# Optimization experiments

Hardware: AMD Instinct MI355X
Metric: run time of the kernel (lower is better)

## Reference

```python
import jax, jax.numpy as jnp
import numpy as np

N_NODES = 50000
N_EDGES = 800000
MAX_ITER = 20  # torchdeq default f_max_iter=40; fixed iteration count for a tractable jit-able baseline
K = 3          # TAGConv default number of hops
INS, EMB, HID, OUT = 4, 64, 128, 1


def setup_inputs():
    key = jax.random.key(0)
    ks = jax.random.split(key, 12)
    def lin(k, fan_in, fan_out):
        return jax.random.normal(k, (fan_in, fan_out), jnp.float32) / np.sqrt(fan_in)
    def tag_w(k, fan_in, fan_out):
        # stacked weights for the K+1 TAGConv linear maps: [K+1, in, out]
        return jax.random.normal(k, (K + 1, fan_in, fan_out), jnp.float32) / np.sqrt(fan_in * (K + 1))
    return {
        "x": jax.random.normal(ks[0], (N_NODES, INS), jnp.float32),
        "pos": jax.random.normal(ks[1], (N_NODES, 3), jnp.float32),
        "edge_attr": jax.random.uniform(ks[2], (N_EDGES,), jnp.float32),
        "up_w1": lin(ks[3], INS, EMB), "up_b1": jnp.zeros((EMB,), jnp.float32),
        "up_w2": lin(ks[4], EMB, EMB), "up_b2": jnp.zeros((EMB,), jnp.float32),
        "c1_w": tag_w(ks[5], EMB + 3, HID), "c1_b": jnp.zeros((HID,), jnp.float32),
        "c2_w": tag_w(ks[6], HID, HID), "c2_b": jnp.zeros((HID,), jnp.float32),
        "c3_w": tag_w(ks[7], HID, EMB), "c3_b": jnp.zeros((EMB,), jnp.float32),
        "down_w1": lin(ks[8], EMB, OUT), "down_b1": jnp.zeros((OUT,), jnp.float32),
        "down_w2": lin(ks[9], OUT, OUT), "down_b2": jnp.zeros((OUT,), jnp.float32),
        "edge_index": jax.random.randint(ks[10], (2, N_EDGES), 0, N_NODES, jnp.int32),
    }


def _gcn_norm(row, col, edge_attr, n):
    # PyG gcn_norm with edge weights, no self loops (TAGConv default)
    deg = jax.ops.segment_sum(edge_attr, col, num_segments=n)
    safe = jnp.where(deg > 0, deg, 1.0)
    dinv = jnp.where(deg > 0, jax.lax.rsqrt(safe), 0.0)
    return dinv[row] * edge_attr * dinv[col]


def _mlp(x, w1, b1, w2, b2):
    # torch F.gelu default = exact erf gelu
    return jax.nn.gelu(x @ w1 + b1, approximate=False) @ w2 + b2


def reference(x, pos, edge_attr, up_w1, up_b1, up_w2, up_b2, c1_w, c1_b, c2_w, c2_b, c3_w, c3_b, down_w1, down_b1, down_w2, down_b2, edge_index):
    n = x.shape[0]
    row, col = edge_index[0], edge_index[1]
    norm = _gcn_norm(row, col, edge_attr, n)

    def tag(h, W, b):
        # TAGConv: sum_k lin_k( A_hat^k x ) + bias
        out = h @ W[0]
        for k in range(1, W.shape[0]):
            h = jax.ops.segment_sum(h[row] * norm[:, None], col, num_segments=n)  # [E,C] gather-scatter
            out = out + h @ W[k]
        return out + b

    def gnn(z):
        h = jnp.concatenate([z, pos], axis=1)
        h = jax.nn.relu(tag(h, c1_w, c1_b))
        h = jax.nn.relu(tag(h, c2_w, c2_b))  # F.dropout is identity in eval mode
        h = tag(h, c3_w, c3_b)
        return jax.nn.log_softmax(h, axis=1)

    z0 = _mlp(x, up_w1, up_b1, up_w2, up_b2)
    z = jax.lax.fori_loop(0, MAX_ITER, lambda i, zz: gnn(zz), z0)  # fixed-point solver
    z_star = gnn(z)  # phantom-gradient step (torchdeq grad=1)
    out = _mlp(z_star, down_w1, down_b1, down_w2, down_b2)
    return out, z_star
```

## Files before the change

kernel.cpp:

```cpp
#include <hip/hip_runtime.h>
#include <hip/hip_bf16.h>

#define N_NODES 50000
#define N_EDGES 800000
#define MAX_ITER 20

typedef __attribute__((ext_vector_type(8))) short bf16x8;
typedef __attribute__((ext_vector_type(4))) float f32x4;
typedef __attribute__((ext_vector_type(2))) float f32x2;
typedef unsigned char uchar;

__device__ __forceinline__ float gelu_f(float x){
  return 0.5f*x*(1.0f+erff(x*0.70710678118654752f));
}
__device__ __forceinline__ ushort f2b(float f){
  uint x = __float_as_uint(f);
  uint r = (x + 0x7fffu + ((x>>16)&1u)) >> 16;
  return (ushort)r;
}

#if __has_builtin(__builtin_amdgcn_cvt_pk_f32_fp8) && __has_builtin(__builtin_amdgcn_cvt_pk_fp8_f32)
#define HW_FP8 1
#endif

__device__ __forceinline__ uint fp8_enc1_sw(float x){
  uint u = __float_as_uint(x);
  uint s = (u>>24)&0x80u;
  int e = (int)((u>>23)&0xffu);
  uint m = u&0x7fffffu;
  uint m3 = (m + 0x80000u)>>20;
  if (m3==8u){ e+=1; m3=0u; }
  int e8 = e-120;
  if (e8<=0) return s;
  if (e8>=15) return s|0x7eu;
  return s | ((uint)e8<<3) | m3;
}
__device__ __forceinline__ float fp8_dec1_sw(uint b){
  uint s=(b&0x80u)<<24;
  uint em=b&0x7fu;
  if (em==0u) return __uint_as_float(s);
  if ((em>>3)==0u) return (s?-1.f:1.f)*(float)em*0.001953125f;
  return __uint_as_float(s | ((em+960u)<<20));
}
__device__ __forceinline__ void fp8_dec8(uint lo, uint hi, float* d){
#ifdef HW_FP8
  f32x2 a = __builtin_amdgcn_cvt_pk_f32_fp8(lo,false);
  f32x2 b = __builtin_amdgcn_cvt_pk_f32_fp8(lo,true);
  f32x2 c = __builtin_amdgcn_cvt_pk_f32_fp8(hi,false);
  f32x2 e = __builtin_amdgcn_cvt_pk_f32_fp8(hi,true);
  d[0]=a[0];d[1]=a[1];d[2]=b[0];d[3]=b[1];d[4]=c[0];d[5]=c[1];d[6]=e[0];d[7]=e[1];
#else
  d[0]=fp8_dec1_sw(lo&0xffu);        d[1]=fp8_dec1_sw((lo>>8)&0xffu);
  d[2]=fp8_dec1_sw((lo>>16)&0xffu);  d[3]=fp8_dec1_sw(lo>>24);
  d[4]=fp8_dec1_sw(hi&0xffu);        d[5]=fp8_dec1_sw((hi>>8)&0xffu);
// ... 128 lines not shown
  float acc2 = sb2[c];
  #pragma unroll 8
  for (int k=0;k<64;k++) acc2 += t1s[g][k]*sw2[k*64+c];
  z[(size_t)node*64+c] = f2b(acc2);
  z8[(size_t)node*64+c] = fp8_enc1(acc2);
}

template<int LDIN>
__global__ void posprop(const float* __restrict__ in, float* __restrict__ out,
                        const int* __restrict__ starts, const int* __restrict__ crow,
                        const float* __restrict__ cnrm){
  int v = blockIdx.x*256+threadIdx.x;
  if (v >= N_NODES) return;
  int s=starts[v], e=starts[v+1];
  float a0=0.f,a1=0.f,a2=0.f;
  for (int i=s;i<e;++i){
    int r=crow[i]; float nm=cnrm[i];
    a0 = fmaf(in[(size_t)r*LDIN+0], nm, a0);
    a1 = fmaf(in[(size_t)r*LDIN+1], nm, a1);
    a2 = fmaf(in[(size_t)r*LDIN+2], nm, a2);
  }
  float4 o = {a0,a1,a2,0.f};
  *(float4*)(out + (size_t)v*4) = o;
}

__global__ __launch_bounds__(256) void posbias_kernel(
    const float* __restrict__ pos, const float* __restrict__ P1,
    const float* __restrict__ P2, const float* __restrict__ P3,
    const float* __restrict__ c1w, const float* __restrict__ c1b,
    ushort* __restrict__ pb){
  __shared__ float sw[4][3][128];
  int tid=threadIdx.x;
  for (int i=tid; i<4*3*128; i+=256){
    int cc=i&127; int d=(i>>7)%3; int j=i/(3*128);
    sw[j][d][cc] = c1w[((size_t)j*67 + 64 + d)*128 + cc];
  }
  __syncthreads();
  int idx = blockIdx.x*256+tid;
  if (idx < N_NODES*128){
    int n = idx>>7, cc = idx&127;
    float a = c1b[cc];
    #pragma unroll
    for (int d=0;d<3;d++) a = fmaf(pos[(size_t)n*3+d], sw[0][d][cc], a);
    #pragma unroll
    for (int d=0;d<3;d++) a = fmaf(P1[(size_t)n*4+d], sw[1][d][cc], a);
    #pragma unroll
    for (int d=0;d<3;d++) a = fmaf(P2[(size_t)n*4+d], sw[2][d][cc], a);
    #pragma unroll
    for (int d=0;d<3;d++) a = fmaf(P3[(size_t)n*4+d], sw[3][d][cc], a);
    pb[idx]=f2b(a);
  }
}

template<int MODE, bool IN8, bool OUT8>
__global__ __launch_bounds__(256) void prop64k(
    const void* __restrict__ hin, ushort* __restrict__ obf,
    uchar* __restrict__ of8, float* __restrict__ of32,
    const ushort* __restrict__ adj, const float* __restrict__ bias,
    const int* __restrict__ starts, const int* __restrict__ crow,
    const float* __restrict__ cnrm){
  constexpr bool WBF = (MODE==0) || (MODE==2) || (MODE==1 && !OUT8);
  int wv = threadIdx.x >> 6;
  int v = blockIdx.x*4 + wv;
  int t = threadIdx.x & 63;
  int g = t >> 3;
  int c = t & 7;
  int s = starts[v], e = starts[v+1];
  float acc[8] = {0,0,0,0,0,0,0,0};
  for (int i=s; i<e; i+=64){
    int cnt = e - i; if (cnt > 64) cnt = 64;
    int r = 0; float nm = 0.f;
    if (t < cnt){ r = crow[i+t]; nm = cnrm[i+t]; }
    for (int jb=0; jb<cnt; jb+=8){
      int rr = __shfl(r, jb+g, 64);
      float nmj = __shfl(nm, jb+g, 64);
      float hv[8];
      if (IN8){
        uint2 d = *(const uint2*)((const uchar*)hin + (size_t)rr*64 + c*8);
        fp8_dec8(d.x, d.y, hv);
      } else {
        uint4 d = *(const uint4*)((const ushort*)hin + (size_t)rr*64 + c*8);
        const uint* dp = (const uint*)&d;
        #pragma unroll
        for (int q=0;q<4;q++){
          hv[2*q]   = __uint_as_float(dp[q]<<16);
          hv[2*q+1] = __uint_as_float(dp[q]&0xffff0000u);
        }
      }
      #pragma unroll
      for (int q=0;q<8;q++) acc[q] = fmaf(hv[q], nmj, acc[q]);
    }
  }
  #pragma unroll
  for (int q=0;q<8;q++){
    acc[q] += __shfl_xor(acc[q], 8, 64);
    acc[q] += __shfl_xor(acc[q], 16, 64);
    acc[q] += __shfl_xor(acc[q], 32, 64);
  }
  if (MODE==0 || MODE==1){
    if (g==0){
      float val[8];
      if (MODE==1){
        uint4 av = *(const uint4*)(adj + (size_t)v*64 + c*8);
        const uint* ap=(const uint*)&av;
        #pragma unroll
        for (int q=0;q<4;q++){
          val[2*q]   = acc[2*q]   + __uint_as_float(ap[q]<<16);
          val[2*q+1] = acc[2*q+1] + __uint_as_float(ap[q]&0xffff0000u);
        }
      } else {
        #pragma unroll
        for (int q=0;q<8;q++) val[q]=acc[q];
      }
      if (WBF){
        uint4 o; uint* op=(uint*)&o;
        #pragma unroll
        for (int q=0;q<4;q++) op[q] = (uint)f2b(val[2*q]) | ((uint)f2b(val[2*q+1])<<16);
        *(uint4*)(obf + (size_t)v*64 + c*8) = o;
      }
      if (OUT8){
        uint2 o8;
        o8.x = fp8_enc4(val[0],val[1],val[2],val[3]);
        o8.y = fp8_enc4(val[4],val[5],val[6],val[7]);
        *(uint2*)(of8 + (size_t)v*64 + c*8) = o8;
      }
    }
  } else {
    uint4 av = *(const uint4*)(adj + (size_t)v*64 + c*8);
    const uint* ap=(const uint*)&av;
    float vv[8];
    #pragma unroll
    for (int q=0;q<4;q++){
      vv[2*q]   = acc[2*q]   + __uint_as_float(ap[q]<<16)         + bias[c*8+2*q];
      vv[2*q+1] = acc[2*q+1] + __uint_as_float(ap[q]&0xffff0000u) + bias[c*8+2*q+1];
    }
    float m = vv[0];
    #pragma unroll
    for (int q=1;q<8;q++) m = fmaxf(m, vv[q]);
    m = fmaxf(m, __shfl_xor(m,1,64));
    m = fmaxf(m, __shfl_xor(m,2,64));
    m = fmaxf(m, __shfl_xor(m,4,64));
    float ss = 0.f;
    #pragma unroll
    for (int q=0;q<8;q++) ss += __expf(vv[q]-m);
    ss += __shfl_xor(ss,1,64);
    ss += __shfl_xor(ss,2,64);
    ss += __shfl_xor(ss,4,64);
    float lse = m + __logf(ss);
    if (g==0){
      if (MODE==2){
        uint4 o; uint* op=(uint*)&o;
        #pragma unroll
        for (int q=0;q<4;q++) op[q] = (uint)f2b(vv[2*q]-lse) | ((uint)f2b(vv[2*q+1]-lse)<<16);
        *(uint4*)(obf + (size_t)v*64 + c*8) = o;
        if (OUT8){
          uint2 o8;
          o8.x = fp8_enc4(vv[0]-lse,vv[1]-lse,vv[2]-lse,vv[3]-lse);
          o8.y = fp8_enc4(vv[4]-lse,vv[5]-lse,vv[6]-lse,vv[7]-lse);
          *(uint2*)(of8 + (size_t)v*64 + c*8) = o8;
        }
      } else {
        float* zo = of32 + (size_t)v*64 + c*8;
        float4 o0 = {vv[0]-lse, vv[1]-lse, vv[2]-lse, vv[3]-lse};
        float4 o1 = {vv[4]-lse, vv[5]-lse, vv[6]-lse, vv[7]-lse};
        *(float4*)zo = o0;
        *(float4*)(zo+4) = o1;
      }
    }
  }
}

template<bool IN8, bool OUT8>
__global__ __launch_bounds__(256) void prop128k(
    const void* __restrict__ hin, ushort* __restrict__ obf,
    uchar* __restrict__ of8,
    const int* __restrict__ starts, const int* __restrict__ crow,
    const float* __restrict__ cnrm){
  int wv = threadIdx.x >> 6;
  int v = blockIdx.x*4 + wv;
  int t = threadIdx.x & 63;
  int g = t >> 4;
  int c = t & 15;
  int s = starts[v], e = starts[v+1];
  float acc[8] = {0,0,0,0,0,0,0,0};
  for (int i=s; i<e; i+=64){
    int cnt = e - i; if (cnt > 64) cnt = 64;
    int r = 0; float nm = 0.f;
    if (t < cnt){ r = crow[i+t]; nm = cnrm[i+t]; }
    for (int jb=0; jb<cnt; jb+=4){
      int rr  = __shfl(r,  jb+g, 64);
      float nmj = __shfl(nm, jb+g, 64);
      float hv[8];
      if (IN8){
        uint2 d = *(const uint2*)((const uchar*)hin + (size_t)rr*128 + c*8);
        fp8_dec8(d.x, d.y, hv);
      } else {
        uint4 d = *(const uint4*)((const ushort*)hin + (size_t)rr*128 + c*8);
        const uint* dp = (const uint*)&d;
        #pragma unroll
        for (int q=0;q<4;q++){
          hv[2*q]   = __uint_as_float(dp[q]<<16);
          hv[2*q+1] = __uint_as_float(dp[q]&0xffff0000u);
        }
      }
      #pragma unroll
      for (int q=0;q<8;q++) acc[q] = fmaf(hv[q], nmj, acc[q]);
    }
  }
  #pragma unroll
  for (int q=0;q<8;q++){
    acc[q] += __shfl_xor(acc[q], 16, 64);
    acc[q] += __shfl_xor(acc[q], 32, 64);
  }
  if (g==0){
    uint4 o; uint* op=(uint*)&o;
    #pragma unroll
    for (int q=0;q<4;q++) op[q] = (uint)f2b(acc[2*q]) | ((uint)f2b(acc[2*q+1])<<16);
    *(uint4*)(obf + (size_t)v*128 + c*8) = o;
    if (OUT8){
      uint2 o8;
      o8.x = fp8_enc4(acc[0],acc[1],acc[2],acc[3]);
      o8.y = fp8_enc4(acc[4],acc[5],acc[6],acc[7]);
      *(uint2*)(of8 + (size_t)v*128 + c*8) = o8;
    }
  }
}

template<int KC, bool PERNODE_BIAS, bool OUT8>
__global__ __launch_bounds__(256) void gemm4in(
    const ushort* __restrict__ H0, const ushort* __restrict__ H1,
    const ushort* __restrict__ H2, const ushort* __restrict__ H3,
    const ushort* __restrict__ PB, const void* __restrict__ biasp,
    ushort* __restrict__ out, uchar* __restrict__ out8){
  constexpr int NT = 8;
  constexpr int NKS = KC/32;
  int lane = threadIdx.x & 63;
  int wv   = threadIdx.x >> 6;
  int m0 = blockIdx.x*64 + wv*16;
  int lr = lane & 15, lg = lane >> 4;
  int arow = m0 + lr; if (arow > N_NODES-1) arow = N_NODES-1;
  const ushort* Hs[4] = {H0,H1,H2,H3};
  f32x4 acc[NT];
  #pragma unroll
  for (int t=0;t<NT;t++) acc[t] = (f32x4){0.f,0.f,0.f,0.f};
  #pragma unroll
  for (int j=0;j<4;j++){
    const ushort* Hj  = Hs[j] + (size_t)arow*KC + lg*8;
    const ushort* PBj = PB + (size_t)j*(KC/8)*128*8;
    #pragma unroll
    for (int ks=0; ks<NKS; ks++){
      bf16x8 af = *(const bf16x8*)(Hj + ks*32);
      int kb = ks*4 + lg;
      #pragma unroll
      for (int t=0;t<NT;t++){
        bf16x8 bf = *(const bf16x8*)(PBj + ((size_t)kb*128 + t*16 + lr)*8);
        acc[t] = __builtin_amdgcn_mfma_f32_16x16x32_bf16(af, bf, acc[t], 0, 0, 0);
      }
    }
  }
  #pragma unroll
  for (int t=0;t<NT;t++){
    #pragma unroll
    for (int q=0;q<4;q++){
      int node = m0 + lg*4 + q;
      if (node < N_NODES){
        int col = t*16 + lr;
        float b;
        if (PERNODE_BIAS) b = __uint_as_float(((uint)((const ushort*)biasp)[(size_t)node*128+col])<<16);
        else              b = ((const float*)biasp)[col];
        float vo = fmaxf(acc[t][q] + b, 0.f);
        out[(size_t)node*128 + col] = f2b(vo);
        if (OUT8) out8[(size_t)node*128 + col] = fp8_enc1(vo);
      }
    }
  }
}

__global__ __launch_bounds__(256) void gemm_y(
    const ushort* __restrict__ T2, const ushort* __restrict__ PB,
    ushort* __restrict__ Y, uchar* __restrict__ Y3_8){
  constexpr int NT = 16;
  int lane = threadIdx.x & 63;
  int wv   = threadIdx.x >> 6;
  int m0 = blockIdx.x*64 + wv*16;
  int lr = lane & 15, lg = lane >> 4;
  int arow = m0 + lr; if (arow > N_NODES-1) arow = N_NODES-1;
  f32x4 acc[NT];
  #pragma unroll
  for (int t=0;t<NT;t++) acc[t] = (f32x4){0.f,0.f,0.f,0.f};
  const ushort* Hj = T2 + (size_t)arow*128 + lg*8;
  #pragma unroll
  for (int ks=0; ks<4; ks++){
    bf16x8 af = *(const bf16x8*)(Hj + ks*32);
    int kb = ks*4 + lg;
    #pragma unroll
    for (int t=0;t<NT;t++){
      bf16x8 bf = *(const bf16x8*)(PB + ((size_t)kb*256 + t*16 + lr)*8);
      acc[t] = __builtin_amdgcn_mfma_f32_16x16x32_bf16(af, bf, acc[t], 0, 0, 0);
    }
  }
  #pragma unroll
  for (int t=0;t<NT;t++){
    int n = t*16 + lr;
    int j = n >> 6, cc = n & 63;
    #pragma unroll
    for (int q=0;q<4;q++){
      int node = m0 + lg*4 + q;
      if (node < N_NODES){
        Y[(size_t)j*N_NODES*64 + (size_t)node*64 + cc] = f2b(acc[t][q]);
        if (j==3) Y3_8[(size_t)node*64 + cc] = fp8_enc1(acc[t][q]);
      }
    }
  }
}

__global__ __launch_bounds__(256) void mlp_down_kernel(
    const float* __restrict__ zs, const float* __restrict__ dw1, const float* __restrict__ db1,
    const float* __restrict__ dw2, const float* __restrict__ db2, float* __restrict__ out){
  int node = blockIdx.x*4 + (threadIdx.x>>6);
  int c = threadIdx.x & 63;
  float v = zs[(size_t)node*64+c]*dw1[c];
  #pragma unroll
  for (int off=32; off; off>>=1) v += __shfl_xor(v, off, 64);
  if (c==0) out[node] = gelu_f(v + db1[0]) * dw2[0] + db2[0];
}

extern "C" void kernel_launch(void* const* d_in, const int* in_sizes, int n_in,
                              void* d_out, int out_size, void* d_ws, size_t ws_size,
                              hipStream_t stream){
  const float* x     = (const float*)d_in[0];
  const float* pos   = (const float*)d_in[1];
  const float* eattr = (const float*)d_in[2];
  const float* up_w1 = (const float*)d_in[3];
  const float* up_b1 = (const float*)d_in[4];
  const float* up_w2 = (const float*)d_in[5];
  const float* up_b2 = (const float*)d_in[6];
  const float* c1_w  = (const float*)d_in[7];
  const float* c1_b  = (const float*)d_in[8];
  const float* c2_w  = (const float*)d_in[9];
  const float* c2_b  = (const float*)d_in[10];
  const float* c3_w  = (const float*)d_in[11];
  const float* c3_b  = (const float*)d_in[12];
  const float* dw1   = (const float*)d_in[13];
  const float* db1   = (const float*)d_in[14];
  const float* dw2   = (const float*)d_in[15];
  const float* db2   = (const float*)d_in[16];
  const int*   eidx  = (const int*)d_in[17];
  const int* row = eidx;
  const int* col = eidx + N_EDGES;

  char* wsp = (char*)d_ws;
  size_t off = 0;
  auto alloc = [&](size_t bytes)->char*{
    char* p = wsp + off;
    off = (off + bytes + 255) & ~(size_t)255;
    return p;
  };
  float*  deg    = (float*)alloc((size_t)N_NODES*4);
  int*    cnt    = (int*)  alloc((size_t)N_NODES*4);
  int*    starts = (int*)  alloc((size_t)(N_NODES+1)*4);
  int*    cursor = (int*)  alloc((size_t)N_NODES*4);
  float*  nrm    = (float*)alloc((size_t)N_EDGES*4);
  int*    crow   = (int*)  alloc((size_t)N_EDGES*4);
  float*  cnrm   = (float*)alloc((size_t)N_EDGES*4);
  float*  P1     = (float*)alloc((size_t)N_NODES*4*4);
  float*  P2     = (float*)alloc((size_t)N_NODES*4*4);
  float*  P3     = (float*)alloc((size_t)N_NODES*4*4);
  ushort* pbias  = (ushort*)alloc((size_t)N_NODES*128*2);
  ushort* z      = (ushort*)alloc((size_t)N_NODES*64*2);
  ushort* q1     = (ushort*)alloc((size_t)N_NODES*64*2);
  ushort* q2     = (ushort*)alloc((size_t)N_NODES*64*2);
  ushort* q3     = (ushort*)alloc((size_t)N_NODES*64*2);
  ushort* t1     = (ushort*)alloc((size_t)N_NODES*128*2);
  ushort* p1     = (ushort*)alloc((size_t)N_NODES*128*2);
  ushort* p2     = (ushort*)alloc((size_t)N_NODES*128*2);
  ushort* p3     = (ushort*)alloc((size_t)N_NODES*128*2);
  ushort* t2     = (ushort*)alloc((size_t)N_NODES*128*2);
  ushort* PB1    = (ushort*)alloc((size_t)4*8*128*8*2);
  ushort* PB2    = (ushort*)alloc((size_t)4*16*128*8*2);
  ushort* PB3    = (ushort*)alloc((size_t)16*256*8*2);
  uchar*  z8     = (uchar*)alloc((size_t)N_NODES*64);
  uchar*  q1_8   = (uchar*)alloc((size_t)N_NODES*64);
  uchar*  q2_8   = (uchar*)alloc((size_t)N_NODES*64);
  uchar*  t1_8   = (uchar*)alloc((size_t)N_NODES*128);
  uchar*  p1_8   = (uchar*)alloc((size_t)N_NODES*128);
  uchar*  p2_8   = (uchar*)alloc((size_t)N_NODES*128);
  uchar*  Y3_8   = (uchar*)alloc((size_t)N_NODES*64);
  uchar*  u1_8   = (uchar*)alloc((size_t)N_NODES*64);
  uchar*  u2_8   = (uchar*)alloc((size_t)N_NODES*64);

  ushort* Y  = p1;
  ushort* Y0 = Y;
  ushort* Y1 = Y + (size_t)1*N_NODES*64;
  ushort* Y2 = Y + (size_t)2*N_NODES*64;
  ushort* Y3 = Y + (size_t)3*N_NODES*64;
  ushort* u1 = q1;
  ushort* u2 = q2;

  float* outv  = (float*)d_out;
  float* zstar = (float*)d_out + N_NODES;

  hipMemsetAsync(deg, 0, (size_t)N_NODES*4, stream);
  hipMemsetAsync(cnt, 0, (size_t)N_NODES*4, stream);
  int eb = (N_EDGES+255)/256;
  deg_cnt_kernel<<<eb,256,0,stream>>>(col, eattr, deg, cnt);
  norm_kernel<<<eb,256,0,stream>>>(row, col, eattr, deg, nrm);
  scan_kernel<<<1,1024,0,stream>>>(cnt, starts, cursor);
  fill_kernel<<<eb,256,0,stream>>>(row, col, nrm, cursor, crow, cnrm);
  pack_w1<<<128,256,0,stream>>>(c1_w, PB1);
  pack_w2<<<256,256,0,stream>>>(c2_w, PB2);
  pack_w3<<<128,256,0,stream>>>(c3_w, PB3);
  mlp_up_kernel<<<N_NODES/4,256,0,stream>>>(x, up_w1, up_b1, up_w2, up_b2, z, z8);

  int nb = (N_NODES+255)/256;
  posprop<3><<<nb,256,0,stream>>>(pos, P1, starts, crow, cnrm);
  posprop<4><<<nb,256,0,stream>>>(P1,  P2, starts, crow, cnrm);
  posprop<4><<<nb,256,0,stream>>>(P2,  P3, starts, crow, cnrm);
  posbias_kernel<<<(N_NODES*128)/256,256,0,stream>>>(pos, P1, P2, P3, c1_w, c1_b, pbias);

  const int gprop = N_NODES/4;
  const int ggemm = (N_NODES+63)/64;

  for (int it=0; it<=MAX_ITER; ++it){
    if (it < MAX_ITER){
      prop64k<0,true,true> <<<gprop,256,0,stream>>>(z8,   q1, q1_8, nullptr, nullptr, nullptr, starts, crow, cnrm);
      prop64k<0,true,true> <<<gprop,256,0,stream>>>(q1_8, q2, q2_8, nullptr, nullptr, nullptr, starts, crow, cnrm);
      prop64k<0,true,false><<<gprop,256,0,stream>>>(q2_8, q3, nullptr, nullptr, nullptr, nullptr, starts, crow, cnrm);
      gemm4in<64,true,true><<<ggemm,256,0,stream>>>(z,q1,q2,q3,PB1,pbias,t1,t1_8);

      prop128k<true,true> <<<gprop,256,0,stream>>>(t1_8, p1, p1_8, starts, crow, cnrm);
      prop128k<true,true> <<<gprop,256,0,stream>>>(p1_8, p2, p2_8, starts, crow, cnrm);
      prop128k<true,false><<<gprop,256,0,stream>>>(p2_8, p3, nullptr, starts, crow, cnrm);
      gemm4in<128,false,false><<<ggemm,256,0,stream>>>(t1,p1,p2,p3,PB2,c2_b,t2,nullptr);

      gemm_y<<<ggemm,256,0,stream>>>(t2, PB3, Y, Y3_8);
      prop64k<1,true,true><<<gprop,256,0,stream>>>(Y3_8, nullptr, u1_8, nullptr, Y2, nullptr, starts, crow, cnrm);
      prop64k<1,true,true><<<gprop,256,0,stream>>>(u1_8, nullptr, u2_8, nullptr, Y1, nullptr, starts, crow, cnrm);
      prop64k<2,true,true><<<gprop,256,0,stream>>>(u2_8, z, z8, nullptr, Y0, c3_b, starts, crow, cnrm);
    } else {
      prop64k<0,false,false><<<gprop,256,0,stream>>>(z,  q1, nullptr, nullptr, nullptr, nullptr, starts, crow, cnrm);
      prop64k<0,false,false><<<gprop,256,0,stream>>>(q1, q2, nullptr, nullptr, nullptr, nullptr, starts, crow, cnrm);
      prop64k<0,false,false><<<gprop,256,0,stream>>>(q2, q3, nullptr, nullptr, nullptr, nullptr, starts, crow, cnrm);
      gemm4in<64,true,false><<<ggemm,256,0,stream>>>(z,q1,q2,q3,PB1,pbias,t1,nullptr);

      prop128k<false,false><<<gprop,256,0,stream>>>(t1, p1, nullptr, starts, crow, cnrm);
      prop128k<false,false><<<gprop,256,0,stream>>>(p1, p2, nullptr, starts, crow, cnrm);
      prop128k<false,false><<<gprop,256,0,stream>>>(p2, p3, nullptr, starts, crow, cnrm);
      gemm4in<128,false,false><<<ggemm,256,0,stream>>>(t1,p1,p2,p3,PB2,c2_b,t2,nullptr);

      gemm_y<<<ggemm,256,0,stream>>>(t2, PB3, Y, Y3_8);
      prop64k<1,false,false><<<gprop,256,0,stream>>>(Y3, u1, nullptr, nullptr, Y2, nullptr, starts, crow, cnrm);
      prop64k<1,false,false><<<gprop,256,0,stream>>>(u1, u2, nullptr, nullptr, Y1, nullptr, starts, crow, cnrm);
      prop64k<3,false,false><<<gprop,256,0,stream>>>(u2, nullptr, nullptr, zstar, Y0, c3_b, starts, crow, cnrm);
    }
  }
  mlp_down_kernel<<<N_NODES/4,256,0,stream>>>(zstar, dw1, db1, dw2, db2, outv);
}
```

Before: 6.940 ms.

## Fuse fixed-point iteration into a persistent cooperative megakernel with grid syncs

Replaces the 252 per-stage kernel launches of the fixed-point loop with one cooperative persistent kernel. Each stage becomes a grid-stride device function, and grid.sync() separates the stages, so launch gaps and tail effects between kernels should go away. The grid is capped at 1024 blocks, fewer than the original per-stage grids, so each block loops over several node groups. Occupancy is limited by the register use of the largest fused body, and grid-wide barriers have their own cost. Falls back to separate launches if the cooperative launch fails.

```diff
diff --git a/kernel.cpp b/kernel.cpp
--- a/kernel.cpp
+++ b/kernel.cpp
@@ -1,5 +1,8 @@
 #include <hip/hip_runtime.h>
 #include <hip/hip_bf16.h>
+#include <hip/hip_cooperative_groups.h>
+
+namespace cg = cooperative_groups;
 
 #define N_NODES 50000
 #define N_EDGES 800000
@@ -234,268 +237,6 @@
   }
 }
 
-template<int MODE, bool IN8, bool OUT8>
-__global__ __launch_bounds__(256) void prop64k(
-    const void* __restrict__ hin, ushort* __restrict__ obf,
-    uchar* __restrict__ of8, float* __restrict__ of32,
-    const ushort* __restrict__ adj, const float* __restrict__ bias,
-    const int* __restrict__ starts, const int* __restrict__ crow,
-    const float* __restrict__ cnrm){
-  constexpr bool WBF = (MODE==0) || (MODE==2) || (MODE==1 && !OUT8);
-  int wv = threadIdx.x >> 6;
-  int v = blockIdx.x*4 + wv;
-  int t = threadIdx.x & 63;
-  int g = t >> 3;
-  int c = t & 7;
-  int s = starts[v], e = starts[v+1];
-  float acc[8] = {0,0,0,0,0,0,0,0};
-  for (int i=s; i<e; i+=64){
-    int cnt = e - i; if (cnt > 64) cnt = 64;
-    int r = 0; float nm = 0.f;
-    if (t < cnt){ r = crow[i+t]; nm = cnrm[i+t]; }
-    for (int jb=0; jb<cnt; jb+=8){
-      int rr = __shfl(r, jb+g, 64);
-      float nmj = __shfl(nm, jb+g, 64);
-      float hv[8];
-      if (IN8){
-        uint2 d = *(const uint2*)((const uchar*)hin + (size_t)rr*64 + c*8);
-        fp8_dec8(d.x, d.y, hv);
-      } else {
-        uint4 d = *(const uint4*)((const ushort*)hin + (size_t)rr*64 + c*8);
-        const uint* dp = (const uint*)&d;
-        #pragma unroll
-        for (int q=0;q<4;q++){
-          hv[2*q]   = __uint_as_float(dp[q]<<16);
-          hv[2*q+1] = __uint_as_float(dp[q]&0xffff0000u);
-        }
-      }
-      #pragma unroll
-      for (int q=0;q<8;q++) acc[q] = fmaf(hv[q], nmj, acc[q]);
-    }
-  }
-  #pragma unroll
-  for (int q=0;q<8;q++){
-    acc[q] += __shfl_xor(acc[q], 8, 64);
-    acc[q] += __shfl_xor(acc[q], 16, 64);
-    acc[q] += __shfl_xor(acc[q], 32, 64);
-  }
-  if (MODE==0 || MODE==1){
-    if (g==0){
-      float val[8];
-      if (MODE==1){
-        uint4 av = *(const uint4*)(adj + (size_t)v*64 + c*8);
-        const uint* ap=(const uint*)&av;
-        #pragma unroll
-        for (int q=0;q<4;q++){
-          val[2*q]   = acc[2*q]   + __uint_as_float(ap[q]<<16);
-          val[2*q+1] = acc[2*q+1] + __uint_as_float(ap[q]&0xffff0000u);
-        }
-      } else {
-        #pragma unroll
-        for (int q=0;q<8;q++) val[q]=acc[q];
-      }
-      if (WBF){
-        uint4 o; uint* op=(uint*)&o;
-        #pragma unroll
-        for (int q=0;q<4;q++) op[q] = (uint)f2b(val[2*q]) | ((uint)f2b(val[2*q+1])<<16);
-        *(uint4*)(obf + (size_t)v*64 + c*8) = o;
-      }
-      if (OUT8){
-        uint2 o8;
-        o8.x = fp8_enc4(val[0],val[1],val[2],val[3]);
-        o8.y = fp8_enc4(val[4],val[5],val[6],val[7]);
-        *(uint2*)(of8 + (size_t)v*64 + c*8) = o8;
-      }
-    }
-  } else {
-    uint4 av = *(const uint4*)(adj + (size_t)v*64 + c*8);
-    const uint* ap=(const uint*)&av;
-    float vv[8];
-    #pragma unroll
-    for (int q=0;q<4;q++){
-      vv[2*q]   = acc[2*q]   + __uint_as_float(ap[q]<<16)         + bias[c*8+2*q];
-      vv[2*q+1] = acc[2*q+1] + __uint_as_float(ap[q]&0xffff0000u) + bias[c*8+2*q+1];
-    }
-    float m = vv[0];
-    #pragma unroll
-    for (int q=1;q<8;q++) m = fmaxf(m, vv[q]);
-    m = fmaxf(m, __shfl_xor(m,1,64));
-    m = fmaxf(m, __shfl_xor(m,2,64));
-    m = fmaxf(m, __shfl_xor(m,4,64));
-    float ss = 0.f;
-    #pragma unroll
-    for (int q=0;q<8;q++) ss += __expf(vv[q]-m);
-    ss += __shfl_xor(ss,1,64);
-    ss += __shfl_xor(ss,2,64);
-    ss += __shfl_xor(ss,4,64);
-    float lse = m + __logf(ss);
-    if (g==0){
-      if (MODE==2){
-        uint4 o; uint* op=(uint*)&o;
-        #pragma unroll
-        for (int q=0;q<4;q++) op[q] = (uint)f2b(vv[2*q]-lse) | ((uint)f2b(vv[2*q+1]-lse)<<16);
-        *(uint4*)(obf + (size_t)v*64 + c*8) = o;
-        if (OUT8){
-          uint2 o8;
-          o8.x = fp8_enc4(vv[0]-lse,vv[1]-lse,vv[2]-lse,vv[3]-lse);
-          o8.y = fp8_enc4(vv[4]-lse,vv[5]-lse,vv[6]-lse,vv[7]-lse);
-          *(uint2*)(of8 + (size_t)v*64 + c*8) = o8;
-        }
-      } else {
-        float* zo = of32 + (size_t)v*64 + c*8;
-        float4 o0 = {vv[0]-lse, vv[1]-lse, vv[2]-lse, vv[3]-lse};
-        float4 o1 = {vv[4]-lse, vv[5]-lse, vv[6]-lse, vv[7]-lse};
-        *(float4*)zo = o0;
-        *(float4*)(zo+4) = o1;
-      }
-    }
-  }
-}
-
-template<bool IN8, bool OUT8>
-__global__ __launch_bounds__(256) void prop128k(
-    const void* __restrict__ hin, ushort* __restrict__ obf,
-    uchar* __restrict__ of8,
-    const int* __restrict__ starts, const int* __restrict__ crow,
-    const float* __restrict__ cnrm){
-  int wv = threadIdx.x >> 6;
-  int v = blockIdx.x*4 + wv;
-  int t = threadIdx.x & 63;
-  int g = t >> 4;
-  int c = t & 15;
-  int s = starts[v], e = starts[v+1];
-  float acc[8] = {0,0,0,0,0,0,0,0};
-  for (int i=s; i<e; i+=64){
-    int cnt = e - i; if (cnt > 64) cnt = 64;
-    int r = 0; float nm = 0.f;
-    if (t < cnt){ r = crow[i+t]; nm = cnrm[i+t]; }
-    for (int jb=0; jb<cnt; jb+=4){
-      int rr  = __shfl(r,  jb+g, 64);
-      float nmj = __shfl(nm, jb+g, 64);
-      float hv[8];
-      if (IN8){
-        uint2 d = *(const uint2*)((const uchar*)hin + (size_t)rr*128 + c*8);
-        fp8_dec8(d.x, d.y, hv);
-      } else {
-        uint4 d = *(const uint4*)((const ushort*)hin + (size_t)rr*128 + c*8);
-        const uint* dp = (const uint*)&d;
-        #pragma unroll
-        for (int q=0;q<4;q++){
-          hv[2*q]   = __uint_as_float(dp[q]<<16);
-          hv[2*q+1] = __uint_as_float(dp[q]&0xffff0000u);
-        }
-      }
-      #pragma unroll
-      for (int q=0;q<8;q++) acc[q] = fmaf(hv[q], nmj, acc[q]);
-    }
-  }
-  #pragma unroll
-  for (int q=0;q<8;q++){
-    acc[q] += __shfl_xor(acc[q], 16, 64);
-    acc[q] += __shfl_xor(acc[q], 32, 64);
-  }
-  if (g==0){
-    uint4 o; uint* op=(uint*)&o;
-    #pragma unroll
-    for (int q=0;q<4;q++) op[q] = (uint)f2b(acc[2*q]) | ((uint)f2b(acc[2*q+1])<<16);
-    *(uint4*)(obf + (size_t)v*128 + c*8) = o;
-    if (OUT8){
-      uint2 o8;
-      o8.x = fp8_enc4(acc[0],acc[1],acc[2],acc[3]);
-      o8.y = fp8_enc4(acc[4],acc[5],acc[6],acc[7]);
-      *(uint2*)(of8 + (size_t)v*128 + c*8) = o8;
-    }
-  }
-}
-
-template<int KC, bool PERNODE_BIAS, bool OUT8>
-__global__ __launch_bounds__(256) void gemm4in(
-    const ushort* __restrict__ H0, const ushort* __restrict__ H1,
-    const ushort* __restrict__ H2, const ushort* __restrict__ H3,
-    const ushort* __restrict__ PB, const void* __restrict__ biasp,
-    ushort* __restrict__ out, uchar* __restrict__ out8){
-  constexpr int NT = 8;
-  constexpr int NKS = KC/32;
-  int lane = threadIdx.x & 63;
-  int wv   = threadIdx.x >> 6;
-  int m0 = blockIdx.x*64 + wv*16;
-  int lr = lane & 15, lg = lane >> 4;
-  int arow = m0 + lr; if (arow > N_NODES-1) arow = N_NODES-1;
-  const ushort* Hs[4] = {H0,H1,H2,H3};
-  f32x4 acc[NT];
-  #pragma unroll
-  for (int t=0;t<NT;t++) acc[t] = (f32x4){0.f,0.f,0.f,0.f};
-  #pragma unroll
-  for (int j=0;j<4;j++){
-    const ushort* Hj  = Hs[j] + (size_t)arow*KC + lg*8;
-    const ushort* PBj = PB + (size_t)j*(KC/8)*128*8;
-    #pragma unroll
-    for (int ks=0; ks<NKS; ks++){
-      bf16x8 af = *(const bf16x8*)(Hj + ks*32);
-      int kb = ks*4 + lg;
-      #pragma unroll
-      for (int t=0;t<NT;t++){
-        bf16x8 bf = *(const bf16x8*)(PBj + ((size_t)kb*128 + t*16 + lr)*8);
-        acc[t] = __builtin_amdgcn_mfma_f32_16x16x32_bf16(af, bf, acc[t], 0, 0, 0);
-      }
-    }
-  }
-  #pragma unroll
-  for (int t=0;t<NT;t++){
-    #pragma unroll
-    for (int q=0;q<4;q++){
-      int node = m0 + lg*4 + q;
-      if (node < N_NODES){
-        int col = t*16 + lr;
-        float b;
-        if (PERNODE_BIAS) b = __uint_as_float(((uint)((const ushort*)biasp)[(size_t)node*128+col])<<16);
-        else              b = ((const float*)biasp)[col];
-        float vo = fmaxf(acc[t][q] + b, 0.f);
-        out[(size_t)node*128 + col] = f2b(vo);
-        if (OUT8) out8[(size_t)node*128 + col] = fp8_enc1(vo);
-      }
-    }
-  }
-}
-
-__global__ __launch_bounds__(256) void gemm_y(
-    const ushort* __restrict__ T2, const ushort* __restrict__ PB,
-    ushort* __restrict__ Y, uchar* __restrict__ Y3_8){
-  constexpr int NT = 16;
-  int lane = threadIdx.x & 63;
-  int wv   = threadIdx.x >> 6;
-  int m0 = blockIdx.x*64 + wv*16;
-  int lr = lane & 15, lg = lane >> 4;
-  int arow = m0 + lr; if (arow > N_NODES-1) arow = N_NODES-1;
-  f32x4 acc[NT];
-  #pragma unroll
-  for (int t=0;t<NT;t++) acc[t] = (f32x4){0.f,0.f,0.f,0.f};
-  const ushort* Hj = T2 + (size_t)arow*128 + lg*8;
-  #pragma unroll
-  for (int ks=0; ks<4; ks++){
-    bf16x8 af = *(const bf16x8*)(Hj + ks*32);
-    int kb = ks*4 + lg;
-    #pragma unroll
-    for (int t=0;t<NT;t++){
-      bf16x8 bf = *(const bf16x8*)(PB + ((size_t)kb*256 + t*16 + lr)*8);
-      acc[t] = __builtin_amdgcn_mfma_f32_16x16x32_bf16(af, bf, acc[t], 0, 0, 0);
-    }
-  }
-  #pragma unroll
-  for (int t=0;t<NT;t++){
-    int n = t*16 + lr;
-    int j = n >> 6, cc = n & 63;
-    #pragma unroll
-    for (int q=0;q<4;q++){
-      int node = m0 + lg*4 + q;
-      if (node < N_NODES){
-        Y[(size_t)j*N_NODES*64 + (size_t)node*64 + cc] = f2b(acc[t][q]);
-        if (j==3) Y3_8[(size_t)node*64 + cc] = fp8_enc1(acc[t][q]);
-      }
-    }
-  }
-}
-
 __global__ __launch_bounds__(256) void mlp_down_kernel(
     const float* __restrict__ zs, const float* __restrict__ dw1, const float* __restrict__ db1,
     const float* __restrict__ dw2, const float* __restrict__ db2, float* __restrict__ out){
@@ -505,6 +246,358 @@
   #pragma unroll
   for (int off=32; off; off>>=1) v += __shfl_xor(v, off, 64);
   if (c==0) out[node] = gelu_f(v + db1[0]) * dw2[0] + db2[0];
+}
+
+
+template<int MODE, bool IN8, bool OUT8>
+__device__ void prop64_body(
+    const void* __restrict__ hin, ushort* __restrict__ obf,
+    uchar* __restrict__ of8, float* __restrict__ of32,
+    const ushort* __restrict__ adj, const float* __restrict__ bias,
+    const int* __restrict__ starts, const int* __restrict__ crow,
+    const float* __restrict__ cnrm){
+  constexpr bool WBF = (MODE==0) || (MODE==2) || (MODE==1 && !OUT8);
+  int wv = threadIdx.x >> 6;
+  int t = threadIdx.x & 63;
+  int g = t >> 3;
+  int c = t & 7;
+  for (int vb = blockIdx.x; vb < N_NODES/4; vb += gridDim.x){
+    int v = vb*4 + wv;
+    int s = starts[v], e = starts[v+1];
+    float acc[8] = {0,0,0,0,0,0,0,0};
+    for (int i=s; i<e; i+=64){
+      int cnt = e - i; if (cnt > 64) cnt = 64;
+      int r = 0; float nm = 0.f;
+      if (t < cnt){ r = crow[i+t]; nm = cnrm[i+t]; }
+      for (int jb=0; jb<cnt; jb+=8){
+        int rr = __shfl(r, jb+g, 64);
+        float nmj = __shfl(nm, jb+g, 64);
+        float hv[8];
+        if (IN8){
+          uint2 d = *(const uint2*)((const uchar*)hin + (size_t)rr*64 + c*8);
+          fp8_dec8(d.x, d.y, hv);
+        } else {
+          uint4 d = *(const uint4*)((const ushort*)hin + (size_t)rr*64 + c*8);
+          const uint* dp = (const uint*)&d;
+          #pragma unroll
+          for (int q=0;q<4;q++){
+            hv[2*q]   = __uint_as_float(dp[q]<<16);
+            hv[2*q+1] = __uint_as_float(dp[q]&0xffff0000u);
+          }
+        }
+        #pragma unroll
+        for (int q=0;q<8;q++) acc[q] = fmaf(hv[q], nmj, acc[q]);
+      }
+    }
+    #pragma unroll
+    for (int q=0;q<8;q++){
+      acc[q] += __shfl_xor(acc[q], 8, 64);
+      acc[q] += __shfl_xor(acc[q], 16, 64);
+      acc[q] += __shfl_xor(acc[q], 32, 64);
+    }
+    if (MODE==0 || MODE==1){
+      if (g==0){
+        float val[8];
+        if (MODE==1){
+          uint4 av = *(const uint4*)(adj + (size_t)v*64 + c*8);
+          const uint* ap=(const uint*)&av;
+          #pragma unroll
+          for (int q=0;q<4;q++){
+            val[2*q]   = acc[2*q]   + __uint_as_float(ap[q]<<16);
+            val[2*q+1] = acc[2*q+1] + __uint_as_float(ap[q]&0xffff0000u);
+          }
+        } else {
+          #pragma unroll
+          for (int q=0;q<8;q++) val[q]=acc[q];
+        }
+        if (WBF){
+          uint4 o; uint* op=(uint*)&o;
+          #pragma unroll
+          for (int q=0;q<4;q++) op[q] = (uint)f2b(val[2*q]) | ((uint)f2b(val[2*q+1])<<16);
+          *(uint4*)(obf + (size_t)v*64 + c*8) = o;
+        }
+        if (OUT8){
+          uint2 o8;
+          o8.x = fp8_enc4(val[0],val[1],val[2],val[3]);
+          o8.y = fp8_enc4(val[4],val[5],val[6],val[7]);
+          *(uint2*)(of8 + (size_t)v*64 + c*8) = o8;
+        }
+      }
+    } else {
+      uint4 av = *(const uint4*)(adj + (size_t)v*64 + c*8);
+      const uint* ap=(const uint*)&av;
+      float vv[8];
+      #pragma unroll
+      for (int q=0;q<4;q++){
+        vv[2*q]   = acc[2*q]   + __uint_as_float(ap[q]<<16)         + bias[c*8+2*q];
+        vv[2*q+1] = acc[2*q+1] + __uint_as_float(ap[q]&0xffff0000u) + bias[c*8+2*q+1];
+      }
+      float m = vv[0];
+      #pragma unroll
+      for (int q=1;q<8;q++) m = fmaxf(m, vv[q]);
+      m = fmaxf(m, __shfl_xor(m,1,64));
+      m = fmaxf(m, __shfl_xor(m,2,64));
+      m = fmaxf(m, __shfl_xor(m,4,64));
+      float ss = 0.f;
+      #pragma unroll
+      for (int q=0;q<8;q++) ss += __expf(vv[q]-m);
+      ss += __shfl_xor(ss,1,64);
+      ss += __shfl_xor(ss,2,64);
+      ss += __shfl_xor(ss,4,64);
+      float lse = m + __logf(ss);
+      if (g==0){
+        if (MODE==2){
+          uint4 o; uint* op=(uint*)&o;
+          #pragma unroll
+          for (int q=0;q<4;q++) op[q] = (uint)f2b(vv[2*q]-lse) | ((uint)f2b(vv[2*q+1]-lse)<<16);
+          *(uint4*)(obf + (size_t)v*64 + c*8) = o;
+          if (OUT8){
+            uint2 o8;
+            o8.x = fp8_enc4(vv[0]-lse,vv[1]-lse,vv[2]-lse,vv[3]-lse);
+            o8.y = fp8_enc4(vv[4]-lse,vv[5]-lse,vv[6]-lse,vv[7]-lse);
+            *(uint2*)(of8 + (size_t)v*64 + c*8) = o8;
+          }
+        } else {
+          float* zo = of32 + (size_t)v*64 + c*8;
+          float4 o0 = {vv[0]-lse, vv[1]-lse, vv[2]-lse, vv[3]-lse};
+          float4 o1 = {vv[4]-lse, vv[5]-lse, vv[6]-lse, vv[7]-lse};
+          *(float4*)zo = o0;
+          *(float4*)(zo+4) = o1;
+        }
+      }
+    }
+  }
+}
+
+template<bool IN8, bool OUT8>
+__device__ void prop128_body(
+    const void* __restrict__ hin, ushort* __restrict__ obf,
+    uchar* __restrict__ of8,
+    const int* __restrict__ starts, const int* __restrict__ crow,
+    const float* __restrict__ cnrm){
+  int wv = threadIdx.x >> 6;
+  int t = threadIdx.x & 63;
+  int g = t >> 4;
+  int c = t & 15;
+  for (int vb = blockIdx.x; vb < N_NODES/4; vb += gridDim.x){
+    int v = vb*4 + wv;
+    int s = starts[v], e = starts[v+1];
+    float acc[8] = {0,0,0,0,0,0,0,0};
+    for (int i=s; i<e; i+=64){
+      int cnt = e - i; if (cnt > 64) cnt = 64;
+      int r = 0; float nm = 0.f;
+      if (t < cnt){ r = crow[i+t]; nm = cnrm[i+t]; }
+      for (int jb=0; jb<cnt; jb+=4){
+        int rr  = __shfl(r,  jb+g, 64);
+        float nmj = __shfl(nm, jb+g, 64);
+        float hv[8];
+        if (IN8){
+          uint2 d = *(const uint2*)((const uchar*)hin + (size_t)rr*128 + c*8);
+          fp8_dec8(d.x, d.y, hv);
+        } else {
+          uint4 d = *(const uint4*)((const ushort*)hin + (size_t)rr*128 + c*8);
+          const uint* dp = (const uint*)&d;
+          #pragma unroll
+          for (int q=0;q<4;q++){
+            hv[2*q]   = __uint_as_float(dp[q]<<16);
+            hv[2*q+1] = __uint_as_float(dp[q]&0xffff0000u);
+          }
+        }
+        #pragma unroll
+        for (int q=0;q<8;q++) acc[q] = fmaf(hv[q], nmj, acc[q]);
+      }
+    }
+    #pragma unroll
+    for (int q=0;q<8;q++){
+      acc[q] += __shfl_xor(acc[q], 16, 64);
+      acc[q] += __shfl_xor(acc[q], 32, 64);
+    }
+    if (g==0){
+      uint4 o; uint* op=(uint*)&o;
+      #pragma unroll
+      for (int q=0;q<4;q++) op[q] = (uint)f2b(acc[2*q]) | ((uint)f2b(acc[2*q+1])<<16);
+      *(uint4*)(obf + (size_t)v*128 + c*8) = o;
+      if (OUT8){
+        uint2 o8;
+        o8.x = fp8_enc4(acc[0],acc[1],acc[2],acc[3]);
+        o8.y = fp8_enc4(acc[4],acc[5],acc[6],acc[7]);
+        *(uint2*)(of8 + (size_t)v*128 + c*8) = o8;
+      }
+    }
+  }
+}
+
+template<int KC, bool PERNODE_BIAS, bool OUT8>
+__device__ void gemm4in_body(
+    const ushort* __restrict__ H0, const ushort* __restrict__ H1,
+    const ushort* __restrict__ H2, const ushort* __restrict__ H3,
+    const ushort* __restrict__ PB, const void* __restrict__ biasp,
+    ushort* __restrict__ out, uchar* __restrict__ out8){
+  constexpr int NT = 8;
+  constexpr int NKS = KC/32;
+  int lane = threadIdx.x & 63;
+  int wv   = threadIdx.x >> 6;
+  int lr = lane & 15, lg = lane >> 4;
+  const ushort* Hs[4] = {H0,H1,H2,H3};
+  for (int tb = blockIdx.x; tb < (N_NODES+63)/64; tb += gridDim.x){
+    int m0 = tb*64 + wv*16;
+    int arow = m0 + lr; if (arow > N_NODES-1) arow = N_NODES-1;
+    f32x4 acc[NT];
+    #pragma unroll
+    for (int t=0;t<NT;t++) acc[t] = (f32x4){0.f,0.f,0.f,0.f};
+    #pragma unroll
+    for (int j=0;j<4;j++){
+      const ushort* Hj  = Hs[j] + (size_t)arow*KC + lg*8;
+      const ushort* PBj = PB + (size_t)j*(KC/8)*128*8;
+      #pragma unroll
+      for (int ks=0; ks<NKS; ks++){
+        bf16x8 af = *(const bf16x8*)(Hj + ks*32);
+        int kb = ks*4 + lg;
+        #pragma unroll
+        for (int t=0;t<NT;t++){
+          bf16x8 bf = *(const bf16x8*)(PBj + ((size_t)kb*128 + t*16 + lr)*8);
+          acc[t] = __builtin_amdgcn_mfma_f32_16x16x32_bf16(af, bf, acc[t], 0, 0, 0);
+        }
+      }
+    }
+    #pragma unroll
+    for (int t=0;t<NT;t++){
+      #pragma unroll
+      for (int q=0;q<4;q++){
+        int node = m0 + lg*4 + q;
+        if (node < N_NODES){
+          int col = t*16 + lr;
+          float b;
+          if (PERNODE_BIAS) b = __uint_as_float(((uint)((const ushort*)biasp)[(size_t)node*128+col])<<16);
+          else              b = ((const float*)biasp)[col];
+          float vo = fmaxf(acc[t][q] + b, 0.f);
+          out[(size_t)node*128 + col] = f2b(vo);
+          if (OUT8) out8[(size_t)node*128 + col] = fp8_enc1(vo);
+        }
+      }
+    }
+  }
+}
+
+__device__ void gemm_y_body(
+    const ushort* __restrict__ T2, const ushort* __restrict__ PB,
+    ushort* __restrict__ Y, uchar* __restrict__ Y3_8){
+  int lane = threadIdx.x & 63;
+  int wv   = threadIdx.x >> 6;
+  int lr = lane & 15, lg = lane >> 4;
+  for (int tb = blockIdx.x; tb < (N_NODES+63)/64; tb += gridDim.x){
+    int m0 = tb*64 + wv*16;
+    int arow = m0 + lr; if (arow > N_NODES-1) arow = N_NODES-1;
+    const ushort* Hj = T2 + (size_t)arow*128 + lg*8;
+    #pragma unroll
+    for (int half=0; half<2; half++){
+      f32x4 acc[8];
+      #pragma unroll
+      for (int t=0;t<8;t++) acc[t] = (f32x4){0.f,0.f,0.f,0.f};
+      #pragma unroll
+      for (int ks=0; ks<4; ks++){
+        bf16x8 af = *(const bf16x8*)(Hj + ks*32);
+        int kb = ks*4 + lg;
+        #pragma unroll
+        for (int t=0;t<8;t++){
+          bf16x8 bf = *(const bf16x8*)(PB + ((size_t)kb*256 + (half*8+t)*16 + lr)*8);
+          acc[t] = __builtin_amdgcn_mfma_f32_16x16x32_bf16(af, bf, acc[t], 0, 0, 0);
+        }
+      }
+      #pragma unroll
+      for (int t=0;t<8;t++){
+        int n = (half*8+t)*16 + lr;
+        int j = n >> 6, cc = n & 63;
+        #pragma unroll
+        for (int q=0;q<4;q++){
+          int node = m0 + lg*4 + q;
+          if (node < N_NODES){
+            Y[(size_t)j*N_NODES*64 + (size_t)node*64 + cc] = f2b(acc[t][q]);
+            if (j==3) Y3_8[(size_t)node*64 + cc] = fp8_enc1(acc[t][q]);
+          }
+        }
+      }
+    }
+  }
+}
+
+template<int MODE, bool IN8, bool OUT8>
+__global__ __launch_bounds__(256) void prop64_k(
+    const void* hin, ushort* obf, uchar* of8, float* of32,
+    const ushort* adj, const float* bias,
+    const int* starts, const int* crow, const float* cnrm){
+  prop64_body<MODE,IN8,OUT8>(hin,obf,of8,of32,adj,bias,starts,crow,cnrm);
+}
+template<bool IN8, bool OUT8>
+__global__ __launch_bounds__(256) void prop128_k(
+    const void* hin, ushort* obf, uchar* of8,
+    const int* starts, const int* crow, const float* cnrm){
+  prop128_body<IN8,OUT8>(hin,obf,of8,starts,crow,cnrm);
+}
+template<int KC, bool PERNODE_BIAS, bool OUT8>
+__global__ __launch_bounds__(256) void gemm4in_k(
+    const ushort* H0, const ushort* H1, const ushort* H2, const ushort* H3,
+    const ushort* PB, const void* biasp, ushort* out, uchar* out8){
+  gemm4in_body<KC,PERNODE_BIAS,OUT8>(H0,H1,H2,H3,PB,biasp,out,out8);
+}
+__global__ __launch_bounds__(256) void gemm_y_k(
+    const ushort* T2, const ushort* PB, ushort* Y, uchar* Y3_8){
+  gemm_y_body(T2,PB,Y,Y3_8);
+}
+
+struct MegaArgs {
+  const int* starts; const int* crow; const float* cnrm;
+  ushort* z; uchar* z8;
+  ushort* q1; ushort* q2; ushort* q3; uchar* q1_8; uchar* q2_8;
+  ushort* t1; uchar* t1_8;
+  ushort* p1; ushort* p2; ushort* p3; uchar* p1_8; uchar* p2_8;
+  ushort* t2;
+  ushort* Y; uchar* Y3_8; uchar* u1_8; uchar* u2_8;
+  ushort* u1; ushort* u2;
+  const ushort* PB1; const ushort* PB2; const ushort* PB3; const ushort* pbias;
+  const float* c2_b; const float* c3_b;
+  float* zstar;
+};
+
+__global__ __launch_bounds__(256, 4) void mega_kernel(MegaArgs a){
+  cg::grid_group grid = cg::this_grid();
+  ushort* Y0 = a.Y;
+  ushort* Y1 = a.Y + (size_t)1*N_NODES*64;
+  ushort* Y2 = a.Y + (size_t)2*N_NODES*64;
+  ushort* Y3 = a.Y + (size_t)3*N_NODES*64;
+  for (int it=0; it<=MAX_ITER; ++it){
+    if (it < MAX_ITER){
+      prop64_body<0,true,true> (a.z8,   a.q1, a.q1_8, nullptr, nullptr, nullptr, a.starts, a.crow, a.cnrm); grid.sync();
+      prop64_body<0,true,true> (a.q1_8, a.q2, a.q2_8, nullptr, nullptr, nullptr, a.starts, a.crow, a.cnrm); grid.sync();
+      prop64_body<0,true,false>(a.q2_8, a.q3, nullptr, nullptr, nullptr, nullptr, a.starts, a.crow, a.cnrm); grid.sync();
+      gemm4in_body<64,true,true>(a.z, a.q1, a.q2, a.q3, a.PB1, a.pbias, a.t1, a.t1_8); grid.sync();
+
+      prop128_body<true,true> (a.t1_8, a.p1, a.p1_8, a.starts, a.crow, a.cnrm); grid.sync();
+      prop128_body<true,true> (a.p1_8, a.p2, a.p2_8, a.starts, a.crow, a.cnrm); grid.sync();
+      prop128_body<true,false>(a.p2_8, a.p3, nullptr, a.starts, a.crow, a.cnrm); grid.sync();
+      gemm4in_body<128,false,false>(a.t1, a.p1, a.p2, a.p3, a.PB2, a.c2_b, a.t2, nullptr); grid.sync();
+
+      gemm_y_body(a.t2, a.PB3, a.Y, a.Y3_8); grid.sync();
+      prop64_body<1,true,true>(a.Y3_8, nullptr, a.u1_8, nullptr, Y2, nullptr, a.starts, a.crow, a.cnrm); grid.sync();
+      prop64_body<1,true,true>(a.u1_8, nullptr, a.u2_8, nullptr, Y1, nullptr, a.starts, a.crow, a.cnrm); grid.sync();
+      prop64_body<2,true,true>(a.u2_8, a.z, a.z8, nullptr, Y0, a.c3_b, a.starts, a.crow, a.cnrm); grid.sync();
+    } else {
+      prop64_body<0,false,false>(a.z,  a.q1, nullptr, nullptr, nullptr, nullptr, a.starts, a.crow, a.cnrm); grid.sync();
+      prop64_body<0,false,false>(a.q1, a.q2, nullptr, nullptr, nullptr, nullptr, a.starts, a.crow, a.cnrm); grid.sync();
+      prop64_body<0,false,false>(a.q2, a.q3, nullptr, nullptr, nullptr, nullptr, a.starts, a.crow, a.cnrm); grid.sync();
+      gemm4in_body<64,true,false>(a.z, a.q1, a.q2, a.q3, a.PB1, a.pbias, a.t1, nullptr); grid.sync();
+
+      prop128_body<false,false>(a.t1, a.p1, nullptr, a.starts, a.crow, a.cnrm); grid.sync();
+      prop128_body<false,false>(a.p1, a.p2, nullptr, a.starts, a.crow, a.cnrm); grid.sync();
+      prop128_body<false,false>(a.p2, a.p3, nullptr, a.starts, a.crow, a.cnrm); grid.sync();
+      gemm4in_body<128,false,false>(a.t1, a.p1, a.p2, a.p3, a.PB2, a.c2_b, a.t2, nullptr); grid.sync();
+
+      gemm_y_body(a.t2, a.PB3, a.Y, a.Y3_8); grid.sync();
+      prop64_body<1,false,false>(Y3, a.u1, nullptr, nullptr, Y2, nullptr, a.starts, a.crow, a.cnrm); grid.sync();
+      prop64_body<1,false,false>(a.u1, a.u2, nullptr, nullptr, Y1, nullptr, a.starts, a.crow, a.cnrm); grid.sync();
+      prop64_body<3,false,false>(a.u2, nullptr, nullptr, a.zstar, Y0, a.c3_b, a.starts, a.crow, a.cnrm);
+    }
+  }
 }
 
 extern "C" void kernel_launch(void* const* d_in, const int* in_sizes, int n_in,
@@ -600,40 +693,67 @@
   posprop<4><<<nb,256,0,stream>>>(P2,  P3, starts, crow, cnrm);
   posbias_kernel<<<(N_NODES*128)/256,256,0,stream>>>(pos, P1, P2, P3, c1_w, c1_b, pbias);
 
-  const int gprop = N_NODES/4;
-  const int ggemm = (N_NODES+63)/64;
-
-  for (int it=0; it<=MAX_ITER; ++it){
-    if (it < MAX_ITER){
-      prop64k<0,true,true> <<<gprop,256,0,stream>>>(z8,   q1, q1_8, nullptr, nullptr, nullptr, starts, crow, cnrm);
-      prop64k<0,true,true> <<<gprop,256,0,stream>>>(q1_8, q2, q2_8, nullptr, nullptr, nullptr, starts, crow, cnrm);
-      prop64k<0,true,false><<<gprop,256,0,stream>>>(q2_8, q3, nullptr, nullptr, nullptr, nullptr, starts, crow, cnrm);
-      gemm4in<64,true,true><<<ggemm,256,0,stream>>>(z,q1,q2,q3,PB1,pbias,t1,t1_8);
-
-      prop128k<true,true> <<<gprop,256,0,stream>>>(t1_8, p1, p1_8, starts, crow, cnrm);
-      prop128k<true,true> <<<gprop,256,0,stream>>>(p1_8, p2, p2_8, starts, crow, cnrm);
-      prop128k<true,false><<<gprop,256,0,stream>>>(p2_8, p3, nullptr, starts, crow, cnrm);
-      gemm4in<128,false,false><<<ggemm,256,0,stream>>>(t1,p1,p2,p3,PB2,c2_b,t2,nullptr);
-
-      gemm_y<<<ggemm,256,0,stream>>>(t2, PB3, Y, Y3_8);
-      prop64k<1,true,true><<<gprop,256,0,stream>>>(Y3_8, nullptr, u1_8, nullptr, Y2, nullptr, starts, crow, cnrm);
-      prop64k<1,true,true><<<gprop,256,0,stream>>>(u1_8, nullptr, u2_8, nullptr, Y1, nullptr, starts, crow, cnrm);
-      prop64k<2,true,true><<<gprop,256,0,stream>>>(u2_8, z, z8, nullptr, Y0, c3_b, starts, crow, cnrm);
-    } else {
-      prop64k<0,false,false><<<gprop,256,0,stream>>>(z,  q1, nullptr, nullptr, nullptr, nullptr, starts, crow, cnrm);
-      prop64k<0,false,false><<<gprop,256,0,stream>>>(q1, q2, nullptr, nullptr, nullptr, nullptr, starts, crow, cnrm);
-      prop64k<0,false,false><<<gprop,256,0,stream>>>(q2, q3, nullptr, nullptr, nullptr, nullptr, starts, crow, cnrm);
-      gemm4in<64,true,false><<<ggemm,256,0,stream>>>(z,q1,q2,q3,PB1,pbias,t1,nullptr);
-
-      prop128k<false,false><<<gprop,256,0,stream>>>(t1, p1, nullptr, starts, crow, cnrm);
-      prop128k<false,false><<<gprop,256,0,stream>>>(p1, p2, nullptr, starts, crow, cnrm);
-      prop128k<false,false><<<gprop,256,0,stream>>>(p2, p3, nullptr, starts, crow, cnrm);
-      gemm4in<128,false,false><<<ggemm,256,0,stream>>>(t1,p1,p2,p3,PB2,c2_b,t2,nullptr);
-
-      gemm_y<<<ggemm,256,0,stream>>>(t2, PB3, Y, Y3_8);
-      prop64k<1,false,false><<<gprop,256,0,stream>>>(Y3, u1, nullptr, nullptr, Y2, nullptr, starts, crow, cnrm);
-      prop64k<1,false,false><<<gprop,256,0,stream>>>(u1, u2, nullptr, nullptr, Y1, nullptr, starts, crow, cnrm);
-      prop64k<3,false,false><<<gprop,256,0,stream>>>(u2, nullptr, nullptr, zstar, Y0, c3_b, starts, crow, cnrm);
+  MegaArgs ma;
+  ma.starts = starts; ma.crow = crow; ma.cnrm = cnrm;
+  ma.z = z; ma.z8 = z8;
+  ma.q1 = q1; ma.q2 = q2; ma.q3 = q3; ma.q1_8 = q1_8; ma.q2_8 = q2_8;
+  ma.t1 = t1; ma.t1_8 = t1_8;
+  ma.p1 = p1; ma.p2 = p2; ma.p3 = p3; ma.p1_8 = p1_8; ma.p2_8 = p2_8;
+  ma.t2 = t2;
+  ma.Y = Y; ma.Y3_8 = Y3_8; ma.u1_8 = u1_8; ma.u2_8 = u2_8;
+  ma.u1 = u1; ma.u2 = u2;
+  ma.PB1 = PB1; ma.PB2 = PB2; ma.PB3 = PB3; ma.pbias = pbias;
+  ma.c2_b = c2_b; ma.c3_b = c3_b;
+  ma.zstar = zstar;
+
+  hipError_t cerr = hipErrorUnknown;
+  int numCU = 0, maxB = 0;
+  int devId = 0;
+  hipGetDevice(&devId);
+  hipDeviceGetAttribute(&numCU, hipDeviceAttributeMultiprocessorCount, devId);
+  hipOccupancyMaxActiveBlocksPerMultiprocessor(&maxB, mega_kernel, 256, 0);
+  int coopGrid = (numCU > 0 && maxB > 0) ? (numCU * maxB) : 0;
+  if (coopGrid > 1024) coopGrid = 1024;
+  if (coopGrid > 0){
+    void* kargs[] = { (void*)&ma };
+    cerr = hipLaunchCooperativeKernel((const void*)mega_kernel, dim3(coopGrid), dim3(256),
+                                      kargs, 0, stream);
+  }
+  if (cerr != hipSuccess){
+    const int gprop = N_NODES/4;
+    const int ggemm = (N_NODES+63)/64;
+    for (int it=0; it<=MAX_ITER; ++it){
+      if (it < MAX_ITER){
+        prop64_k<0,true,true> <<<gprop,256,0,stream>>>(z8,   q1, q1_8, nullptr, nullptr, nullptr, starts, crow, cnrm);
+        prop64_k<0,true,true> <<<gprop,256,0,stream>>>(q1_8, q2, q2_8, nullptr, nullptr, nullptr, starts, crow, cnrm);
+        prop64_k<0,true,false><<<gprop,256,0,stream>>>(q2_8, q3, nullptr, nullptr, nullptr, nullptr, starts, crow, cnrm);
+        gemm4in_k<64,true,true><<<ggemm,256,0,stream>>>(z,q1,q2,q3,PB1,pbias,t1,t1_8);
+
+        prop128_k<true,true> <<<gprop,256,0,stream>>>(t1_8, p1, p1_8, starts, crow, cnrm);
+        prop128_k<true,true> <<<gprop,256,0,stream>>>(p1_8, p2, p2_8, starts, crow, cnrm);
+        prop128_k<true,false><<<gprop,256,0,stream>>>(p2_8, p3, nullptr, starts, crow, cnrm);
+        gemm4in_k<128,false,false><<<ggemm,256,0,stream>>>(t1,p1,p2,p3,PB2,c2_b,t2,nullptr);
+
+        gemm_y_k<<<ggemm,256,0,stream>>>(t2, PB3, Y, Y3_8);
+        prop64_k<1,true,true><<<gprop,256,0,stream>>>(Y3_8, nullptr, u1_8, nullptr, Y2, nullptr, starts, crow, cnrm);
+        prop64_k<1,true,true><<<gprop,256,0,stream>>>(u1_8, nullptr, u2_8, nullptr, Y1, nullptr, starts, crow, cnrm);
+        prop64_k<2,true,true><<<gprop,256,0,stream>>>(u2_8, z, z8, nullptr, Y0, c3_b, starts, crow, cnrm);
+      } else {
+        prop64_k<0,false,false><<<gprop,256,0,stream>>>(z,  q1, nullptr, nullptr, nullptr, nullptr, starts, crow, cnrm);
+        prop64_k<0,false,false><<<gprop,256,0,stream>>>(q1, q2, nullptr, nullptr, nullptr, nullptr, starts, crow, cnrm);
+        prop64_k<0,false,false><<<gprop,256,0,stream>>>(q2, q3, nullptr, nullptr, nullptr, nullptr, starts, crow, cnrm);
+        gemm4in_k<64,true,false><<<ggemm,256,0,stream>>>(z,q1,q2,q3,PB1,pbias,t1,nullptr);
+
+        prop128_k<false,false><<<gprop,256,0,stream>>>(t1, p1, nullptr, starts, crow, cnrm);
+        prop128_k<false,false><<<gprop,256,0,stream>>>(p1, p2, nullptr, starts, crow, cnrm);
+        prop128_k<false,false><<<gprop,256,0,stream>>>(p2, p3, nullptr, starts, crow, cnrm);
+        gemm4in_k<128,false,false><<<ggemm,256,0,stream>>>(t1,p1,p2,p3,PB2,c2_b,t2,nullptr);
+
+        gemm_y_k<<<ggemm,256,0,stream>>>(t2, PB3, Y, Y3_8);
+        prop64_k<1,false,false><<<gprop,256,0,stream>>>(Y3, u1, nullptr, nullptr, Y2, nullptr, starts, crow, cnrm);
+        prop64_k<1,false,false><<<gprop,256,0,stream>>>(u1, u2, nullptr, nullptr, Y1, nullptr, starts, crow, cnrm);
+        prop64_k<3,false,false><<<gprop,256,0,stream>>>(u2, nullptr, nullptr, zstar, Y0, c3_b, starts, crow, cnrm);
+      }
     }
   }
   mlp_down_kernel<<<N_NODES/4,256,0,stream>>>(zstar, dw1, db1, dw2, db2, outv);
```

New measurement: 10.89 ms. 56.8% more time.
